# Optimization experiments

Measured on AMD Instinct MI355X. Metric: run time of the kernel, lower is better.

## Reference

```python
import jax, jax.numpy as jnp
import numpy as np

B, S, IN, META, H, G = 256, 1024, 4, 4, 256, 768  # G = 3*H, gate order (r, z, n)


def setup_inputs() -> dict:
    key = jax.random.key(0)
    ks = jax.random.split(key, 12)
    sc = 1.0 / np.sqrt(H)
    return {
        "x": jax.random.normal(ks[0], (B, S, IN), jnp.float32),
        "meta": jax.random.normal(ks[1], (B, META), jnp.float32),
        "W_ih0": jax.random.normal(ks[2], (G, IN + META), jnp.float32) * sc,
        "W_hh0": jax.random.normal(ks[3], (G, H), jnp.float32) * sc,
        "b_ih0": jax.random.normal(ks[4], (G,), jnp.float32) * sc,
        "b_hh0": jax.random.normal(ks[5], (G,), jnp.float32) * sc,
        "W_ih1": jax.random.normal(ks[6], (G, H), jnp.float32) * sc,
        "W_hh1": jax.random.normal(ks[7], (G, H), jnp.float32) * sc,
        "b_ih1": jax.random.normal(ks[8], (G,), jnp.float32) * sc,
        "b_hh1": jax.random.normal(ks[9], (G,), jnp.float32) * sc,
        "fc_W": jax.random.normal(ks[10], (1, H), jnp.float32) * sc,
        "fc_b": jax.random.normal(ks[11], (1,), jnp.float32) * sc,
    }


def _gru_layer(x_seq, W_ih, W_hh, b_ih, b_hh):
    # x_seq: [B, S, F] -> outputs [B, S, H]. PyTorch GRU, gate order (r, z, n).
    h_dim = W_hh.shape[1]
    # Precompute input projections for all timesteps (one big GEMM).
    xg = jnp.einsum('bsf,gf->sbg', x_seq, W_ih) + b_ih  # [S, B, 3H]

    def step(h, xg_t):
        hg = h @ W_hh.T + b_hh  # [B, 3H]
        r = jax.nn.sigmoid(xg_t[:, :h_dim] + hg[:, :h_dim])
        z = jax.nn.sigmoid(xg_t[:, h_dim:2 * h_dim] + hg[:, h_dim:2 * h_dim])
        n = jnp.tanh(xg_t[:, 2 * h_dim:] + r * hg[:, 2 * h_dim:])
        h_new = (1.0 - z) * n + z * h
        return h_new, h_new

    h0 = jnp.zeros((x_seq.shape[0], h_dim), x_seq.dtype)
    _, out = jax.lax.scan(step, h0, xg)  # out: [S, B, H]
    return jnp.transpose(out, (1, 0, 2))


def reference(x, meta, W_ih0, W_hh0, b_ih0, b_hh0, W_ih1, W_hh1, b_ih1, b_hh1, fc_W, fc_b):
    # Tile meta across time and concat to features: [B, S, IN+META]
    meta_t = jnp.broadcast_to(meta[:, None, :], (x.shape[0], x.shape[1], meta.shape[-1]))
    xin = jnp.concatenate([x, meta_t], axis=-1)
    h1 = _gru_layer(xin, W_ih0, W_hh0, b_ih0, b_hh0)
    h2 = _gru_layer(h1, W_ih1, W_hh1, b_ih1, b_hh1)
    last = h2[:, -1, :]  # [B, H]
    return last @ fc_W.T + fc_b  # [B, 1]
```

## Files before the change

kernel.cpp:

```cpp
#include <hip/hip_runtime.h>
#include <hip/hip_fp16.h>


#define SCH 32
#define NCH 32

typedef _Float16 half8 __attribute__((ext_vector_type(8)));
typedef _Float16 half4_t __attribute__((ext_vector_type(4)));
typedef float f32x4 __attribute__((ext_vector_type(4)));

__device__ __forceinline__ float rcp_(float x) {
#if __has_builtin(__builtin_amdgcn_rcpf)
    return __builtin_amdgcn_rcpf(x);
#else
    return 1.f / x;
#endif
}
__device__ __forceinline__ float exp2_(float x) {
#if __has_builtin(__builtin_amdgcn_exp2f)
    return __builtin_amdgcn_exp2f(x);
#else
    return exp2f(x);
#endif
}
__device__ __forceinline__ float sigf(float v) {
    return rcp_(1.f + exp2_(v * -1.442695041f));
}
__device__ __forceinline__ float tanh_(float v) {
    return 1.f - 2.f * rcp_(1.f + exp2_(v * 2.885390082f));
}

__device__ __forceinline__ void lds_barrier() {
    __asm__ volatile("s_waitcnt lgkmcnt(0)" ::: "memory");
    __builtin_amdgcn_s_barrier();
}

__global__ __launch_bounds__(256) void prep_kernel(
    const float* __restrict__ Whh0, const float* __restrict__ Whh1,
    const float* __restrict__ Wih1,
    _Float16* __restrict__ Wfrag0, _Float16* __restrict__ Wfrag1,
    _Float16* __restrict__ Wi1frag) {
    int tid = blockIdx.x * 256 + threadIdx.x;
    int mat = tid / 24576;
    int r   = tid % 24576;
    int kt   = r / 3072;
    int rem  = r % 3072;
    int nt   = rem >> 6;
    int lane = rem & 63;
    int n = nt * 16 + (lane & 15);
    int k = kt * 32 + (lane >> 4) * 8;
    const float* src = (mat == 0 ? Whh0 : (mat == 1 ? Whh1 : Wih1)) + n * 256 + k;
    _Float16* dst = (mat == 0 ? Wfrag0 : (mat == 1 ? Wfrag1 : Wi1frag)) + (size_t)r * 8;
#pragma unroll
    for (int j = 0; j < 8; j++) dst[j] = (_Float16)src[j];
}

__global__
__attribute__((amdgpu_flat_work_group_size(512, 512), amdgpu_waves_per_eu(2, 2)))
void mega_kernel(
    const float* __restrict__ x, const float* __restrict__ meta,
    const float* __restrict__ Wih0, const float* __restrict__ bih0,
    const float* __restrict__ bhh0,
    const _Float16* __restrict__ Wfrag0, const _Float16* __restrict__ Wfrag1,
    const _Float16* __restrict__ Wi1frag,
    const float* __restrict__ bih1, const float* __restrict__ bhh1,
    float* __restrict__ hst0, float* __restrict__ hst1,
    _Float16* __restrict__ hout0, _Float16* __restrict__ hout1,
    _Float16* __restrict__ xg0a, _Float16* __restrict__ xg0b,
    _Float16* __restrict__ xg1a, _Float16* __restrict__ xg1b,
    const float* __restrict__ fcW, const float* __restrict__ fcb,
    float* __restrict__ out, int k) {
    __shared__ __align__(16) char smem[33792];
    const int bid = blockIdx.x;
    const int tid = threadIdx.x;

    if (bid < 64) {
        const int role = bid >> 5;
        const int cc = role ? k - 2 : k;
        if (cc < 0 || cc >= NCH) return;
        const _Float16* Wfrag = role ? Wfrag1 : Wfrag0;
        const float* bhh      = role ? bhh1 : bhh0;
        const _Float16* xgt   = role ? ((cc & 1) ? xg1b : xg1a)
                                     : ((cc & 1) ? xg0b : xg0a);
        float* hstate         = role ? hst1 : hst0;
        _Float16* hof         = (cc & 1) ? hout1 : hout0;
        const bool doHout = (role == 0);
        const bool doFC   = (role == 1) && (cc == NCH - 1);

        _Float16* shA = (_Float16*)smem;
        float* shred  = (float*)smem;
        const int w = tid >> 6, lane = tid & 63;
        const int lm = lane & 15;
        const int hi = lane >> 5;
        const int blk = bid & 31;

        int nt[6];
        nt[0] = 2 * w;      nt[1] = 2 * w + 1;
        nt[2] = 16 + 2 * w; nt[3] = 17 + 2 * w;
        nt[4] = 32 + 2 * w; nt[5] = 33 + 2 * w;

        half8 Bf[48];
#pragma unroll
        for (int kt = 0; kt < 8; kt++)
#pragma unroll
            for (int t = 0; t < 6; t++)
                Bf[kt * 6 + t] = *(const half8*)(Wfrag + (size_t)((kt * 48 + nt[t]) * 64 + lane) * 8);

        const float bbnA = bhh[512 + 32 * w + lm];
        const float bbnB = bhh[512 + 32 * w + 16 + lm];

        float hreg[4];
        if (cc == 0) {
#pragma unroll
            for (int r = 0; r < 4; r++) hreg[r] = 0.f;
        } else {
            f32x4 v0 = *(const f32x4*)(hstate + ((size_t)(blk * 8 + w) * 64 + lane) * 4);
#pragma unroll
            for (int r = 0; r < 4; r++) hreg[r] = v0[r];
        }

        const int rdo = (lane >> 4) * 64 + (lane & 7) * 8;
        const int wb2 = w * 256 + (hi * 2 + (lm >> 3)) * 64 + ((lane >> 4) & 1) * 32 + (lm & 7);

#pragma unroll
        for (int r = 0; r < 4; r++) shA[wb2 + r * 8] = (_Float16)hreg[r];

        const _Float16* xp = xgt + (size_t)(blk * 8 + w) * 768 + lane * 4;
        _Float16* hop = hof + (size_t)(blk * 8 + w) * 256 + lane * 4;

        half4_t xcb[2][3];
        xcb[0][0] = *(const half4_t*)(xp);
        xcb[0][1] = *(const half4_t*)(xp + 256);
        xcb[0][2] = *(const half4_t*)(xp + 512);
        xp += 196608;

        __syncthreads();

#define GRU_STEP(SIDE)                                                            \
    {                                                                             \
        xcb[(SIDE) ^ 1][0] = *(const half4_t*)(xp);                               \
        xcb[(SIDE) ^ 1][1] = *(const half4_t*)(xp + 256);                         \
        xcb[(SIDE) ^ 1][2] = *(const half4_t*)(xp + 512);                         \
        xp += 196608;                                                             \
        f32x4 acc[6];                                                             \
        acc[0] = acc[1] = acc[2] = acc[3] = (f32x4){0.f, 0.f, 0.f, 0.f};          \
        acc[4] = (f32x4){bbnA, bbnA, bbnA, bbnA};                                 \
        acc[5] = (f32x4){bbnB, bbnB, bbnB, bbnB};                                 \
        _Pragma("unroll")                                                         \
        for (int kt = 0; kt < 8; kt++) {                                          \
            half8 af = *(const half8*)(shA + (SIDE) * 2048 + kt * 256 + rdo);     \
            _Pragma("unroll")                                                     \
            for (int t = 0; t < 6; t++)                                           \
                acc[t] = __builtin_amdgcn_mfma_f32_16x16x32_f16(                  \
                    af, Bf[kt * 6 + t], acc[t], 0, 0, 0);                         \
        }                                                                         \
        f32x4 aR = hi ? acc[1] : acc[0];                                          \
        f32x4 aZ = hi ? acc[3] : acc[2];                                          \
        f32x4 aN = hi ? acc[5] : acc[4];                                          \
        half4_t xR = xcb[SIDE][0];                                                \
        half4_t xZ = xcb[SIDE][1];                                                \
        half4_t xN = xcb[SIDE][2];                                                \
        _Pragma("unroll")                                                         \
        for (int r = 0; r < 4; r++) {                                             \
            float rr = sigf((float)xR[r] + aR[r]);                                \
            float zz = sigf((float)xZ[r] + aZ[r]);                                \
            float nn = tanh_((float)xN[r] + rr * aN[r]);                          \
            hreg[r] = nn + zz * (hreg[r] - nn);                                   \
        }                                                                         \
        _Pragma("unroll")                                                         \
        for (int r = 0; r < 4; r++)                                               \
            shA[((SIDE) ^ 1) * 2048 + wb2 + r * 8] = (_Float16)hreg[r];           \
        if (doHout) {                                                             \
            half4_t hv;                                                           \
            _Pragma("unroll")                                                     \
            for (int r = 0; r < 4; r++) hv[r] = (_Float16)hreg[r];                \
            *(half4_t*)hop = hv;                                                  \
        }                                                                         \
        hop += 65536;                                                             \
        lds_barrier();                                                            \
    }

        for (int s2 = 0; s2 < SCH; s2 += 2) {
            GRU_STEP(0);
            GRU_STEP(1);
        }
#undef GRU_STEP

        {
            f32x4 v0;
#pragma unroll
            for (int r = 0; r < 4; r++) v0[r] = hreg[r];
            *(f32x4*)(hstate + ((size_t)(blk * 8 + w) * 64 + lane) * 4) = v0;
        }

        if (doFC) {
            float fw = fcW[32 * w + hi * 16 + lm];
            f32x4 pv;
#pragma unroll
            for (int r = 0; r < 4; r++) pv[r] = hreg[r] * fw;
            __syncthreads();
            *(f32x4*)(shred + (size_t)(w * 64 + lane) * 4) = pv;
            __syncthreads();
            if (tid < 8) {
                int qq = tid >> 2, rr2 = tid & 3;
                float a = fcb[0];
                for (int ww = 0; ww < 8; ww++)
                    for (int l2 = 0; l2 < 16; l2++)
                        a += shred[(ww * 64 + qq * 16 + l2) * 4 + rr2]
                           + shred[(ww * 64 + 32 + qq * 16 + l2) * 4 + rr2];
                out[blk * 8 + tid] = a;
            }
        }
    } else if (bid < 96) {
        const int cb = k + 1;
        if (cb < 0 || cb >= NCH) return;
        _Float16* xg0 = (cb & 1) ? xg0b : xg0a;
        const int fb = bid - 64;
        float* Wb = (float*)smem;
        for (int i = tid; i < 6912; i += 512)
            Wb[i] = (i < 6144) ? Wih0[i]
                               : (bih0[i - 6144] + ((i - 6144) < 512 ? bhh0[i - 6144] : 0.f));
        __syncthreads();
        const int sub = tid >> 8;
        const int t = tid & 255;
        const int w = t >> 5, l32 = t & 31;
        const int qc = l32 >> 4, lm = l32 & 15;

        float Wr[6][8], br[6];
#pragma unroll
        for (int g3 = 0; g3 < 3; g3++)
#pragma unroll
            for (int tp = 0; tp < 2; tp++) {
                int n = g3 * 256 + 32 * w + 16 * tp + lm;
                int j6 = g3 * 2 + tp;
#pragma unroll
                for (int kk = 0; kk < 8; kk++) Wr[j6][kk] = Wb[n * 8 + kk];
                br[j6] = Wb[6144 + n];
            }
        const int b0 = fb * 8 + qc * 4;
        float4 mv[4];
#pragma unroll
        for (int r = 0; r < 4; r++) mv[r] = *(const float4*)(meta + (b0 + r) * 4);

        for (int sl = 0; sl < 16; sl++) {
            int s_local = sub * 16 + sl;
            int s = cb * SCH + s_local;
            float4 xv[4];
#pragma unroll
            for (int r = 0; r < 4; r++)
                xv[r] = *(const float4*)(x + ((size_t)(b0 + r) * 1024 + s) * 4);
            half4_t o[2][3];
#pragma unroll
            for (int g3 = 0; g3 < 3; g3++)
#pragma unroll
            for (int tp = 0; tp < 2; tp++) {
                    int j6 = g3 * 2 + tp;
#pragma unroll
                    for (int r = 0; r < 4; r++) {
                        float v = br[j6]
                            + xv[r].x * Wr[j6][0] + xv[r].y * Wr[j6][1]
                            + xv[r].z * Wr[j6][2] + xv[r].w * Wr[j6][3]
                            + mv[r].x * Wr[j6][4] + mv[r].y * Wr[j6][5]
                            + mv[r].z * Wr[j6][6] + mv[r].w * Wr[j6][7];
                        o[tp][g3][r] = (_Float16)v;
                    }
                }
            _Float16* dst = xg0 + ((size_t)(s_local * 32 + fb) * 8 + w) * 768;
#pragma unroll
            for (int tp = 0; tp < 2; tp++) {
                int slot4 = (l32 + tp * 32) * 4;
#pragma unroll
                for (int g3 = 0; g3 < 3; g3++)
                    *(half4_t*)(dst + g3 * 256 + slot4) = o[tp][g3];
            }
        }
    } else {
        const int c1 = k - 1;
        if (c1 < 0 || c1 >= NCH) return;
        const _Float16* hof = (c1 & 1) ? hout1 : hout0;
        _Float16* xg1 = (c1 & 1) ? xg1b : xg1a;
        const int fb = bid - 96;
        const int s_ch = fb >> 2;
        const int bb8 = (fb & 3) * 8;
        _Float16* Ah = (_Float16*)smem;

#pragma unroll
        for (int i = 0; i < 8; i++) {
            int u = i * 512 + tid;
            int rq = u >> 8, c = u & 255;
            int blk8 = bb8 + (rq >> 1), qh = rq & 1;
            int wc = c >> 5, hic = (c >> 4) & 1, lmc = c & 15;
            half4_t hv = *(const half4_t*)(hof +
                (((size_t)(s_ch * 32 + blk8) * 8 + wc) * 64 + hic * 32 + qh * 16 + lmc) * 4);
#pragma unroll
            for (int r2 = 0; r2 < 4; r2++)
                Ah[(rq * 4 + r2) * 264 + c] = hv[r2];
        }
        __syncthreads();

        const int th = tid >> 8;
        const int t = tid & 255;
        const int wv = t >> 6, lane = t & 63;
        const int q = lane >> 4, lm = lane & 15;

        float bias[12];
#pragma unroll
        for (int j = 0; j < 12; j++) {
            int n = (wv * 12 + j) * 16 + lm;
            bias[j] = bih1[n] + (n < 512 ? bhh1[n] : 0.f);
        }
        f32x4 acc[2][12] = {};
#pragma unroll
        for (int kt = 0; kt < 8; kt++) {
            half8 af[2], bf[12];
#pragma unroll
            for (int i = 0; i < 2; i++)
                af[i] = *(const half8*)(&Ah[((th * 2 + i) * 16 + lm) * 264 + kt * 32 + q * 8]);
#pragma unroll
            for (int j = 0; j < 12; j++)
                bf[j] = *(const half8*)(Wi1frag + (size_t)((kt * 48 + wv * 12 + j) * 64 + lane) * 8);
#pragma unroll
            for (int i = 0; i < 2; i++)
#pragma unroll
                for (int j = 0; j < 12; j++)
                    acc[i][j] = __builtin_amdgcn_mfma_f32_16x16x32_f16(af[i], bf[j], acc[i][j], 0, 0, 0);
        }
#pragma unroll
        for (int i = 0; i < 2; i++) {
            int tt = fb * 4 + th * 2 + i, s = tt >> 4, bt = tt & 15;
            int blkw = bt * 2 + (q >> 1), qc2 = q & 1;
#pragma unroll
            for (int j = 0; j < 12; j++) {
                int n = (wv * 12 + j) * 16 + lm;
                int g3 = n >> 8, nn = n & 255;
                int wc2 = nn >> 5, tp = (nn >> 4) & 1, lmc2 = nn & 15;
                half4_t v;
#pragma unroll
                for (int r = 0; r < 4; r++) v[r] = (_Float16)(acc[i][j][r] + bias[j]);
                *(half4_t*)(xg1 + ((size_t)(s * 32 + blkw) * 8 + wc2) * 768
                                 + g3 * 256 + (qc2 * 16 + lmc2 + tp * 32) * 4) = v;
            }
        }
    }
}

extern "C" void kernel_launch(void* const* d_in, const int* in_sizes, int n_in,
                              void* d_out, int out_size, void* d_ws, size_t ws_size,
                              hipStream_t stream) {
    const float* x    = (const float*)d_in[0];
    const float* meta = (const float*)d_in[1];
    const float* Wih0 = (const float*)d_in[2];
    const float* Whh0 = (const float*)d_in[3];
    const float* bih0 = (const float*)d_in[4];
    const float* bhh0 = (const float*)d_in[5];
    const float* Wih1 = (const float*)d_in[6];
    const float* Whh1 = (const float*)d_in[7];
    const float* bih1 = (const float*)d_in[8];
    const float* bhh1 = (const float*)d_in[9];
    const float* fcW  = (const float*)d_in[10];
    const float* fcb  = (const float*)d_in[11];
    float* out = (float*)d_out;

    char* ws = (char*)d_ws;
    _Float16* Wfrag0  = (_Float16*)(ws + 0);
    _Float16* Wfrag1  = (_Float16*)(ws + 393216);
    _Float16* Wi1frag = (_Float16*)(ws + 786432);
    float*    hst0    = (float*)(ws + 1179648);
    float*    hst1    = (float*)(ws + 1441792);
    _Float16* hout0   = (_Float16*)(ws + 1703936);
    _Float16* xg0a    = (_Float16*)(ws + 5898240);
    _Float16* xg0b    = (_Float16*)(ws + 18481152);
    _Float16* xg1a    = (_Float16*)(ws + 31064064);
    _Float16* xg1b    = (_Float16*)(ws + 43646976);
    _Float16* hout1   = (_Float16*)(ws + 56229888);

    prep_kernel<<<288, 256, 0, stream>>>(Whh0, Whh1, Wih1, Wfrag0, Wfrag1, Wi1frag);

    for (int k = -1; k <= NCH + 1; k++) {
        mega_kernel<<<224, 512, 0, stream>>>(
            x, meta, Wih0, bih0, bhh0, Wfrag0, Wfrag1, Wi1frag, bih1, bhh1,
            hst0, hst1, hout0, hout1, xg0a, xg0b, xg1a, xg1b, fcW, fcb, out, k);
    }
}
```

Before: 1.491 ms.

## Rotate per-wave K order so own h slice is read before barrier

Each wave now processes the K tiles of the hidden-state matmul in a rotated order that starts with the slice it wrote itself. That slice is read back from shared memory before the barrier, so the first MFMA group can start without waiting on other waves. The weight fragments are loaded in the same rotated order, which also spreads LDS reads across banks between waves. The double-buffered x-gate prefetch is replaced by a single load at the start of each step, which relies on the MFMA work to hide that load's latency.

```diff
diff --git a/kernel.cpp b/kernel.cpp
--- a/kernel.cpp
+++ b/kernel.cpp
@@ -101,10 +101,12 @@
 
         half8 Bf[48];
 #pragma unroll
-        for (int kt = 0; kt < 8; kt++)
+        for (int i = 0; i < 8; i++) {
+            const int p = (w + i) & 7;
 #pragma unroll
             for (int t = 0; t < 6; t++)
-                Bf[kt * 6 + t] = *(const half8*)(Wfrag + (size_t)((kt * 48 + nt[t]) * 64 + lane) * 8);
+                Bf[i * 6 + t] = *(const half8*)(Wfrag + (size_t)((p * 48 + nt[t]) * 64 + lane) * 8);
+        }
 
         const float bbnA = bhh[512 + 32 * w + lm];
         const float bbnB = bhh[512 + 32 * w + 16 + lm];
@@ -120,56 +122,54 @@
         }
 
         const int rdo = (lane >> 4) * 64 + (lane & 7) * 8;
+        const int rdoW = w * 256 + rdo;
         const int wb2 = w * 256 + (hi * 2 + (lm >> 3)) * 64 + ((lane >> 4) & 1) * 32 + (lm & 7);
 
 #pragma unroll
         for (int r = 0; r < 4; r++) shA[wb2 + r * 8] = (_Float16)hreg[r];
+        half8 af0 = *(const half8*)(shA + rdoW);
 
         const _Float16* xp = xgt + (size_t)(blk * 8 + w) * 768 + lane * 4;
         _Float16* hop = hof + (size_t)(blk * 8 + w) * 256 + lane * 4;
 
-        half4_t xcb[2][3];
-        xcb[0][0] = *(const half4_t*)(xp);
-        xcb[0][1] = *(const half4_t*)(xp + 256);
-        xcb[0][2] = *(const half4_t*)(xp + 512);
-        xp += 196608;
+        half4_t xcb[3];
 
         __syncthreads();
 
 #define GRU_STEP(SIDE)                                                            \
     {                                                                             \
-        xcb[(SIDE) ^ 1][0] = *(const half4_t*)(xp);                               \
-        xcb[(SIDE) ^ 1][1] = *(const half4_t*)(xp + 256);                         \
-        xcb[(SIDE) ^ 1][2] = *(const half4_t*)(xp + 512);                         \
+        xcb[0] = *(const half4_t*)(xp);                                           \
+        xcb[1] = *(const half4_t*)(xp + 256);                                     \
+        xcb[2] = *(const half4_t*)(xp + 512);                                     \
         xp += 196608;                                                             \
         f32x4 acc[6];                                                             \
         acc[0] = acc[1] = acc[2] = acc[3] = (f32x4){0.f, 0.f, 0.f, 0.f};          \
         acc[4] = (f32x4){bbnA, bbnA, bbnA, bbnA};                                 \
         acc[5] = (f32x4){bbnB, bbnB, bbnB, bbnB};                                 \
         _Pragma("unroll")                                                         \
-        for (int kt = 0; kt < 8; kt++) {                                          \
-            half8 af = *(const half8*)(shA + (SIDE) * 2048 + kt * 256 + rdo);     \
+        for (int t = 0; t < 6; t++)                                               \
+            acc[t] = __builtin_amdgcn_mfma_f32_16x16x32_f16(                      \
+                af0, Bf[t], acc[t], 0, 0, 0);                                     \
+        _Pragma("unroll")                                                         \
+        for (int i = 1; i < 8; i++) {                                             \
+            half8 af = *(const half8*)(shA + (SIDE) * 2048 +                      \
+                                       (((w + i) & 7) * 256) + rdo);              \
             _Pragma("unroll")                                                     \
             for (int t = 0; t < 6; t++)                                           \
                 acc[t] = __builtin_amdgcn_mfma_f32_16x16x32_f16(                  \
-                    af, Bf[kt * 6 + t], acc[t], 0, 0, 0);                         \
+                    af, Bf[i * 6 + t], acc[t], 0, 0, 0);                          \
         }                                                                         \
         f32x4 aR = hi ? acc[1] : acc[0];                                          \
         f32x4 aZ = hi ? acc[3] : acc[2];                                          \
         f32x4 aN = hi ? acc[5] : acc[4];                                          \
-        half4_t xR = xcb[SIDE][0];                                                \
-        half4_t xZ = xcb[SIDE][1];                                                \
-        half4_t xN = xcb[SIDE][2];                                                \
         _Pragma("unroll")                                                         \
         for (int r = 0; r < 4; r++) {                                             \
-            float rr = sigf((float)xR[r] + aR[r]);                                \
-            float zz = sigf((float)xZ[r] + aZ[r]);                                \
-            float nn = tanh_((float)xN[r] + rr * aN[r]);                          \
+            float rr = sigf((float)xcb[0][r] + aR[r]);                            \
+            float zz = sigf((float)xcb[1][r] + aZ[r]);                            \
+            float nn = tanh_((float)xcb[2][r] + rr * aN[r]);                      \
             hreg[r] = nn + zz * (hreg[r] - nn);                                   \
+            shA[((SIDE) ^ 1) * 2048 + wb2 + r * 8] = (_Float16)hreg[r];           \
         }                                                                         \
-        _Pragma("unroll")                                                         \
-        for (int r = 0; r < 4; r++)                                               \
-            shA[((SIDE) ^ 1) * 2048 + wb2 + r * 8] = (_Float16)hreg[r];           \
         if (doHout) {                                                             \
             half4_t hv;                                                           \
             _Pragma("unroll")                                                     \
@@ -177,6 +177,7 @@
             *(half4_t*)hop = hv;                                                  \
         }                                                                         \
         hop += 65536;                                                             \
+        af0 = *(const half8*)(shA + ((SIDE) ^ 1) * 2048 + rdoW);                  \
         lds_barrier();                                                            \
     }
 
```

New measurement: 2.470 ms. 1.66x slower.
